# Performance work log

Hardware: AMD Instinct MI355X
Metric: run time of the kernel (lower is better)

Reference implementation:

```python
import jax, jax.numpy as jnp
import numpy as np

B, S, N = 1, 128, 256
D_MSA, D_PAIR, D_HID = 256, 128, 32
EPS = 1e-3
LN_EPS = 1e-5


def _layer_norm(x, w, b):
    mu = jnp.mean(x, axis=-1, keepdims=True)
    var = jnp.mean(jnp.square(x - mu), axis=-1, keepdims=True)
    return (x - mu) * jax.lax.rsqrt(var + LN_EPS) * w + b


def setup_inputs() -> dict:
    key = jax.random.key(0)
    ks = jax.random.split(key, 8)
    sc = lambda fan_in: (1.0 / fan_in) ** 0.5
    return {
        "m": jax.random.normal(ks[0], (B, S, N, D_MSA), dtype=jnp.float32),
        "mask": jnp.ones((B, S, N), dtype=jnp.float32),
        "ln_w": jnp.ones((D_MSA,), dtype=jnp.float32),
        "ln_b": jnp.zeros((D_MSA,), dtype=jnp.float32),
        "w1": jax.random.normal(ks[1], (D_HID, D_MSA), dtype=jnp.float32) * sc(D_MSA),
        "b1": jnp.zeros((D_HID,), dtype=jnp.float32),
        "w2": jax.random.normal(ks[2], (D_HID, D_MSA), dtype=jnp.float32) * sc(D_MSA),
        "b2": jnp.zeros((D_HID,), dtype=jnp.float32),
        "w_out": jax.random.normal(ks[3], (D_PAIR, D_HID * D_HID), dtype=jnp.float32) * sc(D_HID * D_HID),
        "b_out": jnp.zeros((D_PAIR,), dtype=jnp.float32),
        "ln_out_w": jnp.ones((D_PAIR,), dtype=jnp.float32),
        "ln_out_b": jnp.zeros((D_PAIR,), dtype=jnp.float32),
        "wz": jax.random.normal(ks[4], (D_PAIR, D_PAIR), dtype=jnp.float32) * sc(D_PAIR),
        "bz": jnp.zeros((D_PAIR,), dtype=jnp.float32),
    }


def reference(m, mask, ln_w, ln_b, w1, b1, w2, b2, w_out, b_out, ln_out_w, ln_out_b, wz, bz):
    # m: [B, S, N, d_msa], mask: [B, S, N]
    x = _layer_norm(m, ln_w, ln_b)
    n_res = mask.shape[-1]
    mk = mask[..., None] * (n_res ** -0.5)          # [B, S, N, 1] (layer_norm_out branch)
    a = (jnp.einsum('bsnd,hd->bsnh', x, w1) + b1) * mk
    b_ = (jnp.einsum('bsnd,hd->bsnh', x, w2) + b2) * mk
    a = jnp.swapaxes(a, -2, -3)                      # [B, N, S, h]
    b_ = jnp.swapaxes(b_, -2, -3)                    # [B, N, S, h]
    outer = jnp.einsum('bisc,bjse->bijce', a, b_)    # [B, N, N, h, h]
    outer = outer.reshape(outer.shape[:-2] + (-1,))  # [B, N, N, h*h]
    z = jnp.einsum('bijk,pk->bijp', outer, w_out) + b_out  # [B, N, N, d_pair]
    norm = jnp.einsum('bsi,bsj->bij', mk[..., 0], mk[..., 0])[..., None]
    z = z / (EPS + norm)
    z = jax.nn.gelu(z, approximate=False)
    z = _layer_norm(z, ln_out_w, ln_out_b)
    z = jnp.einsum('bijp,qp->bijq', z, wz) + bz
    return z
```

## Files before the change

### kernel.cpp

```cpp
#include <hip/hip_runtime.h>
#include <hip/hip_bf16.h>
#include <math.h>

#define EPSC 1e-3f

typedef __attribute__((ext_vector_type(8)))  short  short8;
typedef __attribute__((ext_vector_type(4)))  float  float4v;
typedef __attribute__((ext_vector_type(16))) float  float16v;

static __device__ __forceinline__ unsigned short f2bf(float f) {
    union { float f; unsigned u; } x; x.f = f;
    unsigned r = x.u + 0x7FFFu + ((x.u >> 16) & 1u);
    return (unsigned short)(r >> 16);
}
static __device__ __forceinline__ unsigned pk_bf16(float lo, float hi) {
    union { __hip_bfloat162 h; unsigned u; } cv;
    cv.h = __float22bfloat162_rn(make_float2(lo, hi));
    return cv.u;
}
static __device__ __forceinline__ float4v mfma16(short8 a, short8 b, float4v c) {
    return __builtin_amdgcn_mfma_f32_16x16x32_bf16(a, b, c, 0, 0, 0);
}
static __device__ __forceinline__ float16v mfma32(short8 a, short8 b, float16v c) {
    return __builtin_amdgcn_mfma_f32_32x32x16_bf16(a, b, c, 0, 0, 0);
}

#define OFF_NORM 0ull
#define OFF_AT   262144ull
#define OFF_BT   2359296ull
#define OFF_WOF  4456448ull
#define OFF_WZF  4718592ull

__global__ __launch_bounds__(256) void k_pre(
    const float* __restrict__ m, const float* __restrict__ mask,
    const float* __restrict__ ln_w, const float* __restrict__ ln_b,
    const float* __restrict__ w1, const float* __restrict__ b1,
    const float* __restrict__ w2, const float* __restrict__ b2,
    const float* __restrict__ w_out, const float* __restrict__ wz,
    unsigned short* __restrict__ aT, unsigned short* __restrict__ bT,
    unsigned short* __restrict__ wobF, unsigned short* __restrict__ wzF,
    float* __restrict__ normw)
{
    __shared__ unsigned short xs[64 * 266];
    __shared__ unsigned short tr[64 * 76];
    __shared__ float mkl[64];
    __shared__ float b12[64];
    int t = threadIdx.x;
    int b = blockIdx.x;

    if (b >= 1088) {
        int i = b - 1088, j = t;
        float acc = 0.f;
#pragma unroll 8
        for (int s = 0; s < 128; ++s)
            acc += mask[s * 256 + i] * mask[s * 256 + j];
        normw[i * 256 + j] = acc * (1.0f / 256.0f);
        return;
    }
    if (b >= 512) {
        int idx = (b - 512) * 256 + t;
        if (idx < 131072) {
            int j = idx & 7, lane = (idx >> 3) & 63, k16 = (idx >> 9) & 31;
            int kh = (idx >> 14) & 1, pw = (idx >> 15) & 3;
            int p = pw * 32 + (lane & 31);
            int k = kh * 512 + k16 * 16 + (lane >> 5) * 8 + j;
            wobF[idx] = f2bf(w_out[p * 1024 + k]);
        } else {
            int q = idx - 131072;
            int j = q & 7, lane = (q >> 3) & 63, kk = (q >> 9) & 3, w = q >> 11;
            int p = w * 16 + (lane & 15);
            int k = kk * 32 + (lane >> 4) * 8 + j;
            wzF[q] = f2bf(wz[p * 128 + k]);
        }
        return;
    }

    int w = t >> 6, lane = t & 63;
    int g = lane >> 4, l15 = lane & 15;
    int rr = lane >> 4, l16 = lane & 15;
    int n0 = (b & 31) * 8, s0 = (b >> 5) * 8;

    if (t < 64) {
        b12[t] = (t < 32) ? b1[t] : b2[t - 32];
        mkl[t] = mask[(s0 + (t >> 3)) * 256 + n0 + (t & 7)] * 0.0625f;
    }

    float4 lw4[4], lb4[4];
#pragma unroll
    for (int q = 0; q < 4; ++q) {
        lw4[q] = *(const float4*)(ln_w + q * 64 + l16 * 4);
        lb4[q] = *(const float4*)(ln_b + q * 64 + l16 * 4);
    }

#pragma unroll
    for (int pass = 0; pass < 4; ++pass) {
        int r = w * 16 + pass * 4 + rr;
        const float* src = m + ((size_t)(s0 + (r >> 3)) * 256 + n0 + (r & 7)) * 256;
        float4 v[4];
#pragma unroll
        for (int q = 0; q < 4; ++q)
            v[q] = *(const float4*)(src + q * 64 + l16 * 4);
        float sum = 0.f, sq = 0.f;
#pragma unroll
        for (int q = 0; q < 4; ++q) {
            sum += v[q].x + v[q].y + v[q].z + v[q].w;
            sq  += v[q].x * v[q].x + v[q].y * v[q].y + v[q].z * v[q].z + v[q].w * v[q].w;
        }
#pragma unroll
        for (int mm = 1; mm <= 8; mm <<= 1) {
            sum += __shfl_xor(sum, mm);
            sq  += __shfl_xor(sq, mm);
        }
        float mu = sum * (1.f / 256.f);
        float rstd = rsqrtf(sq * (1.f / 256.f) - mu * mu + 1e-5f);
#pragma unroll
        for (int q = 0; q < 4; ++q) {
            uint2 u;
            u.x = pk_bf16((v[q].x - mu) * rstd * lw4[q].x + lb4[q].x,
                          (v[q].y - mu) * rstd * lw4[q].y + lb4[q].y);
            u.y = pk_bf16((v[q].z - mu) * rstd * lw4[q].z + lb4[q].z,
                          (v[q].w - mu) * rstd * lw4[q].w + lb4[q].w);
            *(uint2*)(xs + r * 266 + q * 64 + l16 * 4) = u;
        }
    }
    __syncthreads();

    float4v zf4 = {0.f, 0.f, 0.f, 0.f};
    float4v acc[4]; acc[0] = zf4; acc[1] = zf4; acc[2] = zf4; acc[3] = zf4;
#pragma unroll
    for (int kk = 0; kk < 8; ++kk) {
        short8 af = *(const short8*)(xs + (w * 16 + l15) * 266 + kk * 32 + g * 8);
#pragma unroll
        for (int ht = 0; ht < 4; ++ht) {
            int h = ht * 16 + l15;
            const float* wr = (h < 32) ? (w1 + h * 256) : (w2 + (h - 32) * 256);
            float4 wa = *(const float4*)(wr + kk * 32 + g * 8);
            float4 wb = *(const float4*)(wr + kk * 32 + g * 8 + 4);
            union { short8 s; unsigned u[4]; } bfr;
            bfr.u[0] = pk_bf16(wa.x, wa.y);
            bfr.u[1] = pk_bf16(wa.z, wa.w);
            bfr.u[2] = pk_bf16(wb.x, wb.y);
            bfr.u[3] = pk_bf16(wb.z, wb.w);
            acc[ht] = mfma16(af, bfr.s, acc[ht]);
        }
    }
#pragma unroll
    for (int ht = 0; ht < 4; ++ht) {
        int h = ht * 16 + l15;
        float bias = b12[h];
        int rbase = w * 16 + g * 4;
        uint2 u;
        u.x = pk_bf16((acc[ht][0] + bias) * mkl[rbase + 0], (acc[ht][1] + bias) * mkl[rbase + 1]);
        u.y = pk_bf16((acc[ht][2] + bias) * mkl[rbase + 2], (acc[ht][3] + bias) * mkl[rbase + 3]);
        *(uint2*)(tr + h * 76 + rbase) = u;
    }
    __syncthreads();

#pragma unroll
    for (int it = 0; it < 2; ++it) {
        int q = t + it * 256;
        int h = q >> 3, n_l = q & 7;
        unsigned short vv[8];
#pragma unroll
        for (int s_l = 0; s_l < 8; ++s_l)
            vv[s_l] = tr[h * 76 + s_l * 8 + n_l];
        uint4 u;
        u.x = (unsigned)vv[0] | ((unsigned)vv[1] << 16);
        u.y = (unsigned)vv[2] | ((unsigned)vv[3] << 16);
        u.z = (unsigned)vv[4] | ((unsigned)vv[5] << 16);
        u.w = (unsigned)vv[6] | ((unsigned)vv[7] << 16);
        int row = n_l * 32 + (h & 31);
        int dwcol = (s0 >> 1) ^ ((row & 7) << 2);
        unsigned short* dst = ((h < 32) ? aT : bT)
            + (size_t)(n0 >> 3) * 32768 + row * 128 + dwcol * 2;
        *(uint4*)dst = u;
    }
}

__global__ __launch_bounds__(512, 2) void k2_fused(
    const unsigned short* __restrict__ aT, const unsigned short* __restrict__ bT,
    const unsigned short* __restrict__ wobF, const unsigned short* __restrict__ wzF,
    const float* __restrict__ b_out, const float* __restrict__ normw,
    const float* __restrict__ ln_ow, const float* __restrict__ ln_ob,
    const float* __restrict__ bz, float* __restrict__ out)
{
    __shared__ char smem[65536];
    unsigned* s32 = (unsigned*)smem;
    unsigned* oL = (unsigned*)smem;
    float* zA = (float*)smem;
    float* zB = (float*)(smem + 16896);
    unsigned short* lnL = (unsigned short*)(smem + 33792);

    int t = threadIdx.x;
    int w = t >> 6, lane = t & 63;
    int g = lane >> 4, l15 = lane & 15;
    int bj = blockIdx.x, bi = blockIdx.y;
    int wn = w & 1, wm = w >> 1;

    const unsigned* Ag = (const unsigned*)(aT + (size_t)bi * 32768);
    const unsigned* Bg = (const unsigned*)(bT + (size_t)bj * 32768);

    float4v zf4 = {0.f, 0.f, 0.f, 0.f};
    float4v acc[4][8];
#pragma unroll
    for (int fm = 0; fm < 4; ++fm)
#pragma unroll
        for (int fn = 0; fn < 8; ++fn) acc[fm][fn] = zf4;

    for (int kh = 0; kh < 2; ++kh) {
        if (kh) __syncthreads();
#pragma unroll
        for (int it = 0; it < 4; ++it) {
            int idx = t + it * 512;
            int row = idx >> 3, c4 = idx & 7;
            int off = (c4 * 4) ^ ((row & 7) << 2);
            *(uint4*)(s32 + row * 32 + off) = *(const uint4*)(Ag + row * 64 + kh * 32 + off);
            *(uint4*)(s32 + 8192 + row * 32 + off) = *(const uint4*)(Bg + row * 64 + kh * 32 + off);
        }
        __syncthreads();
        int sw = (l15 & 7) << 2;
#pragma unroll
        for (int kk2 = 0; kk2 < 2; ++kk2) {
            int col = (kk2 * 16 + g * 4) ^ sw;
            short8 af[4], bf[8];
#pragma unroll
            for (int fm = 0; fm < 4; ++fm)
                af[fm] = *(const short8*)((const char*)(s32 + (wm * 64 + fm * 16 + l15) * 32 + col));
#pragma unroll
            for (int fn = 0; fn < 8; ++fn)
                bf[fn] = *(const short8*)((const char*)(s32 + 8192 + (wn * 128 + fn * 16 + l15) * 32 + col));
#pragma unroll
            for (int fm = 0; fm < 4; ++fm)
#pragma unroll
                for (int fn = 0; fn < 8; ++fn)
                    acc[fm][fn] = mfma16(bf[fn], af[fm], acc[fm][fn]);
        }
    }

    const float4 loA = *(const float4*)(ln_ow + l15 * 8);
    const float4 loB = *(const float4*)(ln_ow + l15 * 8 + 4);
    const float4 lbA = *(const float4*)(ln_ob + l15 * 8);
    const float4 lbB = *(const float4*)(ln_ob + l15 * 8 + 4);
    const float4 boA = *(const float4*)(b_out + l15 * 8);
    const float4 boB = *(const float4*)(b_out + l15 * 8 + 4);
    float lw8[8] = {loA.x, loA.y, loA.z, loA.w, loB.x, loB.y, loB.z, loB.w};
    float lb8[8] = {lbA.x, lbA.y, lbA.z, lbA.w, lbB.x, lbB.y, lbB.z, lbB.w};
    float bo8[8] = {boA.x, boA.y, boA.z, boA.w, boB.x, boB.y, boB.z, boB.w};
    float bzq = bz[w * 16 + l15];

    for (int p = 0; p < 2; ++p) {
        __syncthreads();
        if ((wm >> 1) == p) {
#pragma unroll
            for (int fm = 0; fm < 4; ++fm) {
#pragma unroll
                for (int fn = 0; fn < 8; ++fn) {
                    int pl = ((wm & 1) * 2 + (fm >> 1)) * 8 + wn * 4 + (fn >> 1);
                    int c = (fm & 1) * 16 + l15;
                    int o = (fn & 1) * 8 + 2 * g;
                    int off = c * 16 + o;
                    int dw = pl * 512 + (off ^ ((((pl & 7) ^ (off >> 6)) & 7) << 2));
                    float4v a4 = acc[fm][fn];
                    uint2 u;
                    u.x = pk_bf16(a4[0], a4[1]);
                    u.y = pk_bf16(a4[2], a4[3]);
                    *(uint2*)(oL + dw) = u;
                }
            }
        }
        __syncthreads();

        {
            int kh = w & 1, pw = w >> 1;
            int l31 = lane & 31, h2 = lane >> 5;
            float16v a32 = {0.f};
            const unsigned short* wbase = wobF + (size_t)w * 16384;
#pragma unroll 8
            for (int k16 = 0; k16 < 32; ++k16) {
                int kg = kh * 32 + k16;
                int off = kg * 8 + h2 * 4;
                int dws = off ^ ((((l31 & 7) ^ (off >> 6)) & 7) << 2);
                short8 b2 = *(const short8*)(wbase + (size_t)(k16 * 64 + lane) * 8);
                short8 aA = *(const short8*)(oL + l31 * 512 + dws);
                a32 = mfma32(aA, b2, a32);
            }
            __syncthreads();
            float* zdst = kh ? zB : zA;
#pragma unroll
            for (int reg = 0; reg < 16; ++reg) {
                int pr = (reg & 3) + 8 * (reg >> 2) + 4 * h2;
                zdst[pr * 132 + pw * 32 + l31] = a32[reg];
            }
        }
        __syncthreads();

        {
            int pl = w * 4 + g;
            int iG = bi * 8 + p * 4 + (pl >> 3), jG = bj * 8 + (pl & 7);
            float inv = 1.0f / (EPSC + normw[iG * 256 + jG]);
            float4v zA0 = *(const float4v*)(zA + pl * 132 + l15 * 8);
            float4v zA1 = *(const float4v*)(zA + pl * 132 + l15 * 8 + 4);
            float4v zB0 = *(const float4v*)(zB + pl * 132 + l15 * 8);
            float4v zB1 = *(const float4v*)(zB + pl * 132 + l15 * 8 + 4);
            float vals[8];
            float sum = 0.f, sq = 0.f;
#pragma unroll
            for (int e2 = 0; e2 < 8; ++e2) {
                float v = ((e2 < 4) ? (zA0[e2] + zB0[e2]) : (zA1[e2 - 4] + zB1[e2 - 4])) + bo8[e2];
                v *= inv;
                v = 0.5f * v * (1.0f + erff(v * 0.70710678118654752f));
                vals[e2] = v; sum += v; sq += v * v;
            }
#pragma unroll
            for (int mm = 1; mm <= 8; mm <<= 1) {
                sum += __shfl_xor(sum, mm);
                sq  += __shfl_xor(sq, mm);
            }
            float mu = sum * (1.0f / 128.0f);
            float rstd = rsqrtf(sq * (1.0f / 128.0f) - mu * mu + 1e-5f);
            uint4 upk;
            upk.x = pk_bf16((vals[0] - mu) * rstd * lw8[0] + lb8[0],
                            (vals[1] - mu) * rstd * lw8[1] + lb8[1]);
            upk.y = pk_bf16((vals[2] - mu) * rstd * lw8[2] + lb8[2],
                            (vals[3] - mu) * rstd * lw8[3] + lb8[3]);
            upk.z = pk_bf16((vals[4] - mu) * rstd * lw8[4] + lb8[4],
                            (vals[5] - mu) * rstd * lw8[5] + lb8[5]);
            upk.w = pk_bf16((vals[6] - mu) * rstd * lw8[6] + lb8[6],
                            (vals[7] - mu) * rstd * lw8[7] + lb8[7]);
            *(uint4*)(lnL + pl * 136 + l15 * 8) = upk;
        }
        __syncthreads();

        {
            float4v acc3[2]; acc3[0] = zf4; acc3[1] = zf4;
#pragma unroll
            for (int kk = 0; kk < 4; ++kk) {
                short8 bfw = *(const short8*)(wzF + ((size_t)(w * 4 + kk) * 64 + lane) * 8);
#pragma unroll
                for (int fr = 0; fr < 2; ++fr) {
                    short8 af3 = *(const short8*)(lnL + (fr * 16 + l15) * 136 + kk * 32 + g * 8);
                    acc3[fr] = mfma16(af3, bfw, acc3[fr]);
                }
            }
#pragma unroll
            for (int fr = 0; fr < 2; ++fr) {
#pragma unroll
                for (int r = 0; r < 4; ++r) {
                    int pl = fr * 16 + g * 4 + r;
                    int row = (bi * 8 + p * 4 + (pl >> 3)) * 256 + bj * 8 + (pl & 7);
                    out[(size_t)row * 128 + w * 16 + l15] = acc3[fr][r] + bzq;
                }
            }
        }
    }
}

extern "C" void kernel_launch(void* const* d_in, const int* in_sizes, int n_in,
                              void* d_out, int out_size, void* d_ws, size_t ws_size,
                              hipStream_t stream) {
    const float* m      = (const float*)d_in[0];
    const float* mask   = (const float*)d_in[1];
    const float* ln_w   = (const float*)d_in[2];
    const float* ln_b   = (const float*)d_in[3];
    const float* w1     = (const float*)d_in[4];
    const float* b1     = (const float*)d_in[5];
    const float* w2     = (const float*)d_in[6];
    const float* b2     = (const float*)d_in[7];
    const float* w_out  = (const float*)d_in[8];
    const float* b_out  = (const float*)d_in[9];
    const float* ln_ow  = (const float*)d_in[10];
    const float* ln_ob  = (const float*)d_in[11];
    const float* wz     = (const float*)d_in[12];
    const float* bz     = (const float*)d_in[13];
    float* out = (float*)d_out;
    char*  ws  = (char*)d_ws;

    float* normw          = (float*)(ws + OFF_NORM);
    unsigned short* aTb   = (unsigned short*)(ws + OFF_AT);
    unsigned short* bTb   = (unsigned short*)(ws + OFF_BT);
    unsigned short* wobF  = (unsigned short*)(ws + OFF_WOF);
    unsigned short* wzF   = (unsigned short*)(ws + OFF_WZF);

    k_pre<<<dim3(1344), dim3(256), 0, stream>>>(m, mask, ln_w, ln_b, w1, b1, w2, b2,
                                                w_out, wz, aTb, bTb, wobF, wzF, normw);
    k2_fused<<<dim3(32, 32), dim3(512), 0, stream>>>(aTb, bTb, wobF, wzF, b_out, normw,
                                                     ln_ow, ln_ob, bz, out);
}
```

Before: 188.3 us.

## Process all 64 pairs per block with 1024 threads and full-K LDS staging

Doubles the k2_fused block to 1024 threads and LDS to 128KB. The whole K dimension of the A/B tiles is now loaded into shared memory in one straight copy, and all 64 (i,j) pairs go through the outer-product, w_out projection, GELU/LN and wz stages in a single pass, replacing the old two-pass loop. Each wave now holds a 4x4 fragment accumulator instead of 4x8. This removes the second staging round and several barriers, but it forces one block per CU and makes every barrier span 16 waves, which can lose overlap between blocks.

```diff
diff --git a/kernel.cpp b/kernel.cpp
--- a/kernel.cpp
+++ b/kernel.cpp
@@ -177,179 +177,176 @@
     }
 }
 
-__global__ __launch_bounds__(512, 2) void k2_fused(
+__global__ __launch_bounds__(1024, 4) void k2_fused(
     const unsigned short* __restrict__ aT, const unsigned short* __restrict__ bT,
     const unsigned short* __restrict__ wobF, const unsigned short* __restrict__ wzF,
     const float* __restrict__ b_out, const float* __restrict__ normw,
     const float* __restrict__ ln_ow, const float* __restrict__ ln_ob,
     const float* __restrict__ bz, float* __restrict__ out)
 {
-    __shared__ char smem[65536];
+    __shared__ char smem[131072];
     unsigned* s32 = (unsigned*)smem;
     unsigned* oL = (unsigned*)smem;
     float* zA = (float*)smem;
-    float* zB = (float*)(smem + 16896);
-    unsigned short* lnL = (unsigned short*)(smem + 33792);
+    float* zB = (float*)(smem + 33792);
+    unsigned short* lnL = (unsigned short*)(smem + 67584);
 
     int t = threadIdx.x;
     int w = t >> 6, lane = t & 63;
     int g = lane >> 4, l15 = lane & 15;
     int bj = blockIdx.x, bi = blockIdx.y;
-    int wn = w & 1, wm = w >> 1;
-
-    const unsigned* Ag = (const unsigned*)(aT + (size_t)bi * 32768);
-    const unsigned* Bg = (const unsigned*)(bT + (size_t)bj * 32768);
+    int wm = w >> 2, wn = w & 3;
+
+    {
+        const uint4* Agv = (const uint4*)(aT + (size_t)bi * 32768);
+        const uint4* Bgv = (const uint4*)(bT + (size_t)bj * 32768);
+#pragma unroll
+        for (int it = 0; it < 4; ++it) {
+            int q = t + it * 1024;
+            *(uint4*)(s32 + q * 4) = Agv[q];
+            *(uint4*)(s32 + 16384 + q * 4) = Bgv[q];
+        }
+    }
+    __syncthreads();
 
     float4v zf4 = {0.f, 0.f, 0.f, 0.f};
-    float4v acc[4][8];
+    float4v acc[4][4];
 #pragma unroll
     for (int fm = 0; fm < 4; ++fm)
 #pragma unroll
-        for (int fn = 0; fn < 8; ++fn) acc[fm][fn] = zf4;
-
-    for (int kh = 0; kh < 2; ++kh) {
-        if (kh) __syncthreads();
-#pragma unroll
-        for (int it = 0; it < 4; ++it) {
-            int idx = t + it * 512;
-            int row = idx >> 3, c4 = idx & 7;
-            int off = (c4 * 4) ^ ((row & 7) << 2);
-            *(uint4*)(s32 + row * 32 + off) = *(const uint4*)(Ag + row * 64 + kh * 32 + off);
-            *(uint4*)(s32 + 8192 + row * 32 + off) = *(const uint4*)(Bg + row * 64 + kh * 32 + off);
+        for (int fn = 0; fn < 4; ++fn) acc[fm][fn] = zf4;
+
+    {
+        int sw = (l15 & 7) << 2;
+#pragma unroll
+        for (int kk = 0; kk < 4; ++kk) {
+            int col = (kk * 16 + g * 4) ^ sw;
+            short8 af[4], bf[4];
+#pragma unroll
+            for (int fm = 0; fm < 4; ++fm)
+                af[fm] = *(const short8*)((const char*)(s32 + (wm * 64 + fm * 16 + l15) * 64 + col));
+#pragma unroll
+            for (int fn = 0; fn < 4; ++fn)
+                bf[fn] = *(const short8*)((const char*)(s32 + 16384 + (wn * 64 + fn * 16 + l15) * 64 + col));
+#pragma unroll
+            for (int fm = 0; fm < 4; ++fm)
+#pragma unroll
+                for (int fn = 0; fn < 4; ++fn)
+                    acc[fm][fn] = mfma16(bf[fn], af[fm], acc[fm][fn]);
+        }
+    }
+    __syncthreads();
+
+#pragma unroll
+    for (int fm = 0; fm < 4; ++fm) {
+#pragma unroll
+        for (int fn = 0; fn < 4; ++fn) {
+            int pl = (wm * 2 + (fm >> 1)) * 8 + wn * 2 + (fn >> 1);
+            int c = (fm & 1) * 16 + l15;
+            int o = (fn & 1) * 8 + 2 * g;
+            int off = c * 16 + o;
+            int dw = pl * 512 + (off ^ ((((pl & 7) ^ (off >> 6)) & 7) << 2));
+            float4v a4 = acc[fm][fn];
+            uint2 u;
+            u.x = pk_bf16(a4[0], a4[1]);
+            u.y = pk_bf16(a4[2], a4[3]);
+            *(uint2*)(oL + dw) = u;
+        }
+    }
+    __syncthreads();
+
+    {
+        int pw = w & 3, kh = (w >> 2) & 1, ph = w >> 3;
+        int l31 = lane & 31, h2 = lane >> 5;
+        int pairR = ph * 32 + l31;
+        float16v a32 = {0.f};
+        const unsigned short* wbase = wobF + (size_t)(pw * 2 + kh) * 16384;
+#pragma unroll 8
+        for (int k16 = 0; k16 < 32; ++k16) {
+            int kg = kh * 32 + k16;
+            int off = kg * 8 + h2 * 4;
+            int dws = off ^ ((((pairR & 7) ^ (off >> 6)) & 7) << 2);
+            short8 b2 = *(const short8*)(wbase + (size_t)(k16 * 64 + lane) * 8);
+            short8 aA = *(const short8*)(oL + pairR * 512 + dws);
+            a32 = mfma32(aA, b2, a32);
         }
         __syncthreads();
-        int sw = (l15 & 7) << 2;
-#pragma unroll
-        for (int kk2 = 0; kk2 < 2; ++kk2) {
-            int col = (kk2 * 16 + g * 4) ^ sw;
-            short8 af[4], bf[8];
-#pragma unroll
-            for (int fm = 0; fm < 4; ++fm)
-                af[fm] = *(const short8*)((const char*)(s32 + (wm * 64 + fm * 16 + l15) * 32 + col));
-#pragma unroll
-            for (int fn = 0; fn < 8; ++fn)
-                bf[fn] = *(const short8*)((const char*)(s32 + 8192 + (wn * 128 + fn * 16 + l15) * 32 + col));
-#pragma unroll
-            for (int fm = 0; fm < 4; ++fm)
-#pragma unroll
-                for (int fn = 0; fn < 8; ++fn)
-                    acc[fm][fn] = mfma16(bf[fn], af[fm], acc[fm][fn]);
-        }
-    }
-
-    const float4 loA = *(const float4*)(ln_ow + l15 * 8);
-    const float4 loB = *(const float4*)(ln_ow + l15 * 8 + 4);
-    const float4 lbA = *(const float4*)(ln_ob + l15 * 8);
-    const float4 lbB = *(const float4*)(ln_ob + l15 * 8 + 4);
-    const float4 boA = *(const float4*)(b_out + l15 * 8);
-    const float4 boB = *(const float4*)(b_out + l15 * 8 + 4);
-    float lw8[8] = {loA.x, loA.y, loA.z, loA.w, loB.x, loB.y, loB.z, loB.w};
-    float lb8[8] = {lbA.x, lbA.y, lbA.z, lbA.w, lbB.x, lbB.y, lbB.z, lbB.w};
-    float bo8[8] = {boA.x, boA.y, boA.z, boA.w, boB.x, boB.y, boB.z, boB.w};
-    float bzq = bz[w * 16 + l15];
-
-    for (int p = 0; p < 2; ++p) {
-        __syncthreads();
-        if ((wm >> 1) == p) {
-#pragma unroll
-            for (int fm = 0; fm < 4; ++fm) {
-#pragma unroll
-                for (int fn = 0; fn < 8; ++fn) {
-                    int pl = ((wm & 1) * 2 + (fm >> 1)) * 8 + wn * 4 + (fn >> 1);
-                    int c = (fm & 1) * 16 + l15;
-                    int o = (fn & 1) * 8 + 2 * g;
-                    int off = c * 16 + o;
-                    int dw = pl * 512 + (off ^ ((((pl & 7) ^ (off >> 6)) & 7) << 2));
-                    float4v a4 = acc[fm][fn];
-                    uint2 u;
-                    u.x = pk_bf16(a4[0], a4[1]);
-                    u.y = pk_bf16(a4[2], a4[3]);
-                    *(uint2*)(oL + dw) = u;
-                }
+        float* zdst = kh ? zB : zA;
+#pragma unroll
+        for (int reg = 0; reg < 16; ++reg) {
+            int pr = (reg & 3) + 8 * (reg >> 2) + 4 * h2;
+            zdst[(ph * 32 + pr) * 132 + pw * 32 + l31] = a32[reg];
+        }
+    }
+    __syncthreads();
+
+    {
+        const float4 loA = *(const float4*)(ln_ow + l15 * 8);
+        const float4 loB = *(const float4*)(ln_ow + l15 * 8 + 4);
+        const float4 lbA = *(const float4*)(ln_ob + l15 * 8);
+        const float4 lbB = *(const float4*)(ln_ob + l15 * 8 + 4);
+        const float4 boA = *(const float4*)(b_out + l15 * 8);
+        const float4 boB = *(const float4*)(b_out + l15 * 8 + 4);
+        float lw8[8] = {loA.x, loA.y, loA.z, loA.w, loB.x, loB.y, loB.z, loB.w};
+        float lb8[8] = {lbA.x, lbA.y, lbA.z, lbA.w, lbB.x, lbB.y, lbB.z, lbB.w};
+        float bo8[8] = {boA.x, boA.y, boA.z, boA.w, boB.x, boB.y, boB.z, boB.w};
+
+        int pl = w * 4 + g;
+        int iG = bi * 8 + (pl >> 3), jG = bj * 8 + (pl & 7);
+        float inv = 1.0f / (EPSC + normw[iG * 256 + jG]);
+        float4v zA0 = *(const float4v*)(zA + pl * 132 + l15 * 8);
+        float4v zA1 = *(const float4v*)(zA + pl * 132 + l15 * 8 + 4);
+        float4v zB0 = *(const float4v*)(zB + pl * 132 + l15 * 8);
+        float4v zB1 = *(const float4v*)(zB + pl * 132 + l15 * 8 + 4);
+        float vals[8];
+        float sum = 0.f, sq = 0.f;
+#pragma unroll
+        for (int e2 = 0; e2 < 8; ++e2) {
+            float v = ((e2 < 4) ? (zA0[e2] + zB0[e2]) : (zA1[e2 - 4] + zB1[e2 - 4])) + bo8[e2];
+            v *= inv;
+            v = 0.5f * v * (1.0f + erff(v * 0.70710678118654752f));
+            vals[e2] = v; sum += v; sq += v * v;
+        }
+#pragma unroll
+        for (int mm = 1; mm <= 8; mm <<= 1) {
+            sum += __shfl_xor(sum, mm);
+            sq  += __shfl_xor(sq, mm);
+        }
+        float mu = sum * (1.0f / 128.0f);
+        float rstd = rsqrtf(sq * (1.0f / 128.0f) - mu * mu + 1e-5f);
+        uint4 upk;
+        upk.x = pk_bf16((vals[0] - mu) * rstd * lw8[0] + lb8[0],
+                        (vals[1] - mu) * rstd * lw8[1] + lb8[1]);
+        upk.y = pk_bf16((vals[2] - mu) * rstd * lw8[2] + lb8[2],
+                        (vals[3] - mu) * rstd * lw8[3] + lb8[3]);
+        upk.z = pk_bf16((vals[4] - mu) * rstd * lw8[4] + lb8[4],
+                        (vals[5] - mu) * rstd * lw8[5] + lb8[5]);
+        upk.w = pk_bf16((vals[6] - mu) * rstd * lw8[6] + lb8[6],
+                        (vals[7] - mu) * rstd * lw8[7] + lb8[7]);
+        *(uint4*)(lnL + pl * 136 + l15 * 8) = upk;
+    }
+    __syncthreads();
+
+    {
+        int qw = w & 7, fh = w >> 3;
+        float4v acc3[2]; acc3[0] = zf4; acc3[1] = zf4;
+#pragma unroll
+        for (int kk = 0; kk < 4; ++kk) {
+            short8 bfw = *(const short8*)(wzF + ((size_t)(qw * 4 + kk) * 64 + lane) * 8);
+#pragma unroll
+            for (int fr2 = 0; fr2 < 2; ++fr2) {
+                short8 af3 = *(const short8*)(lnL + ((fh * 2 + fr2) * 16 + l15) * 136 + kk * 32 + g * 8);
+                acc3[fr2] = mfma16(af3, bfw, acc3[fr2]);
             }
         }
-        __syncthreads();
-
-        {
-            int kh = w & 1, pw = w >> 1;
-            int l31 = lane & 31, h2 = lane >> 5;
-            float16v a32 = {0.f};
-            const unsigned short* wbase = wobF + (size_t)w * 16384;
-#pragma unroll 8
-            for (int k16 = 0; k16 < 32; ++k16) {
-                int kg = kh * 32 + k16;
-                int off = kg * 8 + h2 * 4;
-                int dws = off ^ ((((l31 & 7) ^ (off >> 6)) & 7) << 2);
-                short8 b2 = *(const short8*)(wbase + (size_t)(k16 * 64 + lane) * 8);
-                short8 aA = *(const short8*)(oL + l31 * 512 + dws);
-                a32 = mfma32(aA, b2, a32);
-            }
-            __syncthreads();
-            float* zdst = kh ? zB : zA;
-#pragma unroll
-            for (int reg = 0; reg < 16; ++reg) {
-                int pr = (reg & 3) + 8 * (reg >> 2) + 4 * h2;
-                zdst[pr * 132 + pw * 32 + l31] = a32[reg];
-            }
-        }
-        __syncthreads();
-
-        {
-            int pl = w * 4 + g;
-            int iG = bi * 8 + p * 4 + (pl >> 3), jG = bj * 8 + (pl & 7);
-            float inv = 1.0f / (EPSC + normw[iG * 256 + jG]);
-            float4v zA0 = *(const float4v*)(zA + pl * 132 + l15 * 8);
-            float4v zA1 = *(const float4v*)(zA + pl * 132 + l15 * 8 + 4);
-            float4v zB0 = *(const float4v*)(zB + pl * 132 + l15 * 8);
-            float4v zB1 = *(const float4v*)(zB + pl * 132 + l15 * 8 + 4);
-            float vals[8];
-            float sum = 0.f, sq = 0.f;
-#pragma unroll
-            for (int e2 = 0; e2 < 8; ++e2) {
-                float v = ((e2 < 4) ? (zA0[e2] + zB0[e2]) : (zA1[e2 - 4] + zB1[e2 - 4])) + bo8[e2];
-                v *= inv;
-                v = 0.5f * v * (1.0f + erff(v * 0.70710678118654752f));
-                vals[e2] = v; sum += v; sq += v * v;
-            }
-#pragma unroll
-            for (int mm = 1; mm <= 8; mm <<= 1) {
-                sum += __shfl_xor(sum, mm);
-                sq  += __shfl_xor(sq, mm);
-            }
-            float mu = sum * (1.0f / 128.0f);
-            float rstd = rsqrtf(sq * (1.0f / 128.0f) - mu * mu + 1e-5f);
-            uint4 upk;
-            upk.x = pk_bf16((vals[0] - mu) * rstd * lw8[0] + lb8[0],
-                            (vals[1] - mu) * rstd * lw8[1] + lb8[1]);
-            upk.y = pk_bf16((vals[2] - mu) * rstd * lw8[2] + lb8[2],
-                            (vals[3] - mu) * rstd * lw8[3] + lb8[3]);
-            upk.z = pk_bf16((vals[4] - mu) * rstd * lw8[4] + lb8[4],
-                            (vals[5] - mu) * rstd * lw8[5] + lb8[5]);
-            upk.w = pk_bf16((vals[6] - mu) * rstd * lw8[6] + lb8[6],
-                            (vals[7] - mu) * rstd * lw8[7] + lb8[7]);
-            *(uint4*)(lnL + pl * 136 + l15 * 8) = upk;
-        }
-        __syncthreads();
-
-        {
-            float4v acc3[2]; acc3[0] = zf4; acc3[1] = zf4;
-#pragma unroll
-            for (int kk = 0; kk < 4; ++kk) {
-                short8 bfw = *(const short8*)(wzF + ((size_t)(w * 4 + kk) * 64 + lane) * 8);
-#pragma unroll
-                for (int fr = 0; fr < 2; ++fr) {
-                    short8 af3 = *(const short8*)(lnL + (fr * 16 + l15) * 136 + kk * 32 + g * 8);
-                    acc3[fr] = mfma16(af3, bfw, acc3[fr]);
-                }
-            }
-#pragma unroll
-            for (int fr = 0; fr < 2; ++fr) {
-#pragma unroll
-                for (int r = 0; r < 4; ++r) {
-                    int pl = fr * 16 + g * 4 + r;
-                    int row = (bi * 8 + p * 4 + (pl >> 3)) * 256 + bj * 8 + (pl & 7);
-                    out[(size_t)row * 128 + w * 16 + l15] = acc3[fr][r] + bzq;
-                }
+        float bzq = bz[qw * 16 + l15];
+#pragma unroll
+        for (int fr2 = 0; fr2 < 2; ++fr2) {
+#pragma unroll
+            for (int r = 0; r < 4; ++r) {
+                int pair = (fh * 2 + fr2) * 16 + g * 4 + r;
+                int row = (bi * 8 + (pair >> 3)) * 256 + bj * 8 + (pair & 7);
+                out[(size_t)row * 128 + qw * 16 + l15] = acc3[fr2][r] + bzq;
             }
         }
     }
@@ -383,6 +380,6 @@
 
     k_pre<<<dim3(1344), dim3(256), 0, stream>>>(m, mask, ln_w, ln_b, w1, b1, w2, b2,
                                                 w_out, wz, aTb, bTb, wobF, wzF, normw);
-    k2_fused<<<dim3(32, 32), dim3(512), 0, stream>>>(aTb, bTb, wobF, wzF, b_out, normw,
-                                                     ln_ow, ln_ob, bz, out);
-}
+    k2_fused<<<dim3(32, 32), dim3(1024), 0, stream>>>(aTb, bTb, wobF, wzF, b_out, normw,
+                                                      ln_ow, ln_ob, bz, out);
+}
```

New measurement: 176.2 us. 1.07x faster.
